# Kernel optimization log

Hardware: AMD Instinct MI355X
Metric: run time of the kernel (lower is better)

Reference implementation:

```python
import jax, jax.numpy as jnp
import numpy as np
import math

D_INPUT = 1024
D_Q = 1024
D_K = 1024
D_V = 1024
D_MODEL = 1024
B, S = 4, 2048


def setup_inputs() -> dict:
    key = jax.random.key(0)
    ks = jax.random.split(key, 9)
    sc = 0.02
    return {
        "x": jax.random.normal(ks[0], (B, S, D_INPUT), dtype=jnp.float32),
        "wq": jax.random.normal(ks[1], (D_INPUT, D_Q), dtype=jnp.float32) * sc,
        "bq": jnp.zeros((D_Q,), dtype=jnp.float32),
        "wk": jax.random.normal(ks[2], (D_INPUT, D_K), dtype=jnp.float32) * sc,
        "bk": jnp.zeros((D_K,), dtype=jnp.float32),
        "wv": jax.random.normal(ks[3], (D_INPUT, D_V), dtype=jnp.float32) * sc,
        "bv": jnp.zeros((D_V,), dtype=jnp.float32),
        "wp": jax.random.normal(ks[4], (D_V, D_MODEL), dtype=jnp.float32) * sc,
        "bp": jnp.zeros((D_MODEL,), dtype=jnp.float32),
    }


def reference(x, wq, bq, wk, bk, wv, bv, wp, bp):
    scale = math.sqrt(D_K)  # NOTE: original MULTIPLIES by sqrt(d_k)
    q = x @ wq + bq  # [B,S,Dq]
    k = x @ wk + bk  # [B,S,Dk]
    v = x @ wv + bv  # [B,S,Dv]
    scores = jnp.einsum('bsd,btd->bst', q, k) * scale
    p_attn = jax.nn.softmax(scores, axis=-1)
    # dropout: inference mode (training=False) -> identity
    context = jnp.einsum('bst,btd->bsd', p_attn, v)
    output = context @ wp + bp
    return (output, p_attn)
```

## Files before the change

### kernel.cpp

```cpp
#include <hip/hip_runtime.h>

typedef unsigned short u16;
typedef short bf16x8 __attribute__((ext_vector_type(8)));
typedef float floatx4 __attribute__((ext_vector_type(4)));

static __device__ __forceinline__ u16 f2bf(float f) {
  unsigned int u = __float_as_uint(f);
  unsigned int lsb = (u >> 16) & 1u;
  u += 0x7FFFu + lsb;
  return (u16)(u >> 16);
}
static __device__ __forceinline__ float bf2f(u16 u) {
  return __uint_as_float(((unsigned int)u) << 16);
}

static __device__ __forceinline__ void gl_lds16(const u16* g, u16* l) {
  __builtin_amdgcn_global_load_lds(
      (const __attribute__((address_space(1))) void*)g,
      (__attribute__((address_space(3))) void*)l, 16, 0, 0);
}

__global__ __launch_bounds__(256)
void prep_weights(const float* __restrict__ wq, const float* __restrict__ wk,
                  const float* __restrict__ wv, const float* __restrict__ wp,
                  const float* __restrict__ bq, const float* __restrict__ bk,
                  u16* __restrict__ qkvThi, u16* __restrict__ qkvTlo,
                  u16* __restrict__ wpThi, float* __restrict__ bqk) {
  __shared__ float t[32][33];
  const int z = blockIdx.z;
  const int tid = threadIdx.x;
  if (z == 4) {
    if (blockIdx.y == 0 && blockIdx.x < 8) {
      const int i = blockIdx.x * 256 + tid;
      bqk[i] = (i < 1024) ? bq[i] : bk[i - 1024];
    }
    return;
  }
  const float* in = (z == 0) ? wq : (z == 1) ? wk : (z == 2) ? wv : wp;
  u16* hi = (z == 3) ? wpThi : (qkvThi + (size_t)z * 1024 * 1024);
  u16* lo = (z == 0) ? qkvTlo : (z == 1) ? (qkvTlo + 1024 * 1024) : (u16*)nullptr;
  const int want_lo = (z < 2);

  const int r0 = blockIdx.y * 32, c0 = blockIdx.x * 32;
  const int lr = tid >> 3;
  const int lc = (tid & 7) * 4;
  float4 v = *(const float4*)(in + (size_t)(r0 + lr) * 1024 + c0 + lc);
  t[lr][lc + 0] = v.x; t[lr][lc + 1] = v.y; t[lr][lc + 2] = v.z; t[lr][lc + 3] = v.w;
  __syncthreads();
  u16 ph[4], pl[4];
#pragma unroll
  for (int j = 0; j < 4; j++) {
    float f = t[lc + j][lr];
    ph[j] = f2bf(f);
    pl[j] = f2bf(f - bf2f(ph[j]));
  }
  const size_t o = (size_t)(c0 + lr) * 1024 + r0 + lc;
  *(uint2*)(hi + o) = *(uint2*)ph;
  if (want_lo) *(uint2*)(lo + o) = *(uint2*)pl;
}

__global__ __launch_bounds__(256)
void split_f32(const float* __restrict__ in, u16* __restrict__ hi,
               u16* __restrict__ lo) {
  const size_t i4 = ((size_t)blockIdx.x * 256 + threadIdx.x) * 4;
  float4 v = *(const float4*)(in + i4);
  float f[4] = {v.x, v.y, v.z, v.w};
  u16 ph[4], pl[4];
#pragma unroll
  for (int j = 0; j < 4; j++) {
    ph[j] = f2bf(f[j]);
    pl[j] = f2bf(f[j] - bf2f(ph[j]));
  }
  *(uint2*)(hi + i4) = *(uint2*)ph;
  *(uint2*)(lo + i4) = *(uint2*)pl;
}

template<int KB, int ASP, int BSP, int OM, int HB>
__global__ __launch_bounds__(256)
void gemm_mfma(const u16* __restrict__ Ahi, const u16* __restrict__ Alo,
               const u16* __restrict__ Bhi, const u16* __restrict__ Blo,
               const float* __restrict__ bias,
               void* __restrict__ C0, void* __restrict__ C1,
               void* __restrict__ C2, void* __restrict__ C3,
               int N, int K, int lda, int ldb, int ldc,
               long long aB, long long bB, long long cB, float scale) {
  constexpr int CM = KB / 8 - 1;
  constexpr int RPI = 512 / KB;
  constexpr int NI = KB / 16;
  constexpr int PL = 128 * KB;
  __shared__ __align__(16) u16 As[(1 + ASP) * PL];
  __shared__ __align__(16) u16 Bs[(1 + BSP) * PL];

  const int bz = blockIdx.z;
  const u16* A0 = Ahi + (size_t)bz * aB;
  const u16* A1 = ASP ? (Alo + (size_t)bz * aB) : (const u16*)nullptr;
  const u16* B0 = Bhi + (size_t)bz * bB;
  const u16* B1 = BSP ? (Blo + (size_t)bz * bB) : (const u16*)nullptr;

  const int m0 = blockIdx.y * 128;
  const int n0 = blockIdx.x * 128;
  const int tid = threadIdx.x;
  const int w = tid >> 6;
  const int L = tid & 63;
  const int rr = L & 15, quad = L >> 4;
  const int wm = (w >> 1) * 64, wn = (w & 1) * 64;

  const int lrow = (KB == 32) ? (L >> 2) : (L >> 3);
  const int c3 = (L & CM) ^ ((L >> 3) & CM);
  const int srow = w * 32 + lrow;
  u16* stA = &As[w * 32 * KB];
  u16* stB = &Bs[w * 32 * KB];
  const u16* gA0 = A0 + (size_t)(m0 + srow) * lda + c3 * 8;
  const u16* gA1 = ASP ? A1 + (size_t)(m0 + srow) * lda + c3 * 8 : (const u16*)nullptr;
  const u16* gB0 = B0 + (size_t)(n0 + srow) * ldb + c3 * 8;
  const u16* gB1 = BSP ? B1 + (size_t)(n0 + srow) * ldb + c3 * 8 : (const u16*)nullptr;

  floatx4 acc[4][4] = {};

  for (int k0 = 0; k0 < K; k0 += KB) {
#pragma unroll
    for (int q = 0; q < NI; q++) {
      gl_lds16(gA0 + k0 + (size_t)q * RPI * lda, stA + q * 512);
      gl_lds16(gB0 + k0 + (size_t)q * RPI * ldb, stB + q * 512);
    }
    if (ASP) {
#pragma unroll
      for (int q = 0; q < NI; q++)
        gl_lds16(gA1 + k0 + (size_t)q * RPI * lda, stA + PL + q * 512);
    }
    if (BSP) {
#pragma unroll
      for (int q = 0; q < NI; q++)
        gl_lds16(gB1 + k0 + (size_t)q * RPI * ldb, stB + PL + q * 512);
    }
    __syncthreads();

#pragma unroll
    for (int s = 0; s < KB / 32; s++) {
      const int pcb = ((KB == 32) ? (quad ^ ((rr >> 1) & 3))
                                  : ((s * 4 + quad) ^ (rr & 7))) * 8;
      bf16x8 a0[4], a1[4], b0[4], b1[4];
#pragma unroll
      for (int i = 0; i < 4; i++) {
        const int arow = wm + i * 16 + rr;
        const int brow = wn + i * 16 + rr;
        a0[i] = *(const bf16x8*)&As[arow * KB + pcb];
        b0[i] = *(const bf16x8*)&Bs[brow * KB + pcb];
        if (ASP) a1[i] = *(const bf16x8*)&As[PL + arow * KB + pcb];
        if (BSP) b1[i] = *(const bf16x8*)&Bs[PL + brow * KB + pcb];
      }
#pragma unroll
      for (int i = 0; i < 4; i++) {
#pragma unroll
        for (int j = 0; j < 4; j++) {
          acc[i][j] = __builtin_amdgcn_mfma_f32_16x16x32_bf16(a0[i], b0[j], acc[i][j], 0, 0, 0);
          if (ASP && BSP) {
            acc[i][j] = __builtin_amdgcn_mfma_f32_16x16x32_bf16(a0[i], b1[j], acc[i][j], 0, 0, 0);
            acc[i][j] = __builtin_amdgcn_mfma_f32_16x16x32_bf16(a1[i], b0[j], acc[i][j], 0, 0, 0);
          }
        }
      }
    }
    __syncthreads();
  }

#pragma unroll
  for (int i = 0; i < 4; i++) {
    const int mbase = m0 + wm + i * 16 + quad * 4;
#pragma unroll
    for (int j = 0; j < 4; j++) {
      const int col = n0 + wn + j * 16 + rr;
      float bvs = 0.f;
      if (HB) bvs = bias[col];
      if (OM == 3) {
        u16 pk[4];
#pragma unroll
        for (int ii = 0; ii < 4; ii++) pk[ii] = f2bf(acc[i][j][ii] * scale + bvs);
        const size_t idx = (size_t)(mbase >> 11) * (2048 * 1024) +
                           (size_t)col * 2048 + (mbase & 2047);
        *(uint2*)((u16*)C0 + idx) = *(uint2*)pk;
      } else if (OM == 5) {
        u16* hi; u16* lo;
        if (col < 1024) { hi = (u16*)C0; lo = (u16*)C1; }
        else            { hi = (u16*)C2; lo = (u16*)C3; }
        const int cc = col & 1023;
#pragma unroll
        for (int ii = 0; ii < 4; ii++) {
          const float v = acc[i][j][ii] + bvs;
          const size_t idx = (size_t)(mbase + ii) * 1024 + cc;
          const u16 h = f2bf(v);
          hi[idx] = h;
          lo[idx] = f2bf(v - bf2f(h));
        }
      } else {
        u16* Cb = (u16*)C0 + (size_t)bz * cB;
        float* Cf = (float*)C0 + (size_t)bz * cB;
        u16* Cl = (OM == 1) ? ((u16*)C1 + (size_t)bz * cB) : (u16*)nullptr;
#pragma unroll
        for (int ii = 0; ii < 4; ii++) {
          const float v = acc[i][j][ii] * scale + bvs;
          const size_t idx = (size_t)(mbase + ii) * ldc + col;
          if (OM == 0) {
            Cb[idx] = f2bf(v);
          } else if (OM == 1) {
            const u16 h = f2bf(v);
            Cb[idx] = h;
            Cl[idx] = f2bf(v - bf2f(h));
          } else {
            Cf[idx] = v;
          }
        }
      }
    }
  }
}

__global__ __launch_bounds__(256)
void softmax_rows(float* __restrict__ S, u16* __restrict__ Pb) {
  const int row = blockIdx.x;
  float* s = S + (size_t)row * 2048;
  const int tid = threadIdx.x;
  const int w = tid >> 6;
  __shared__ float redm[4];
  __shared__ float reds[4];

  float v[8];
  float mx = -1e30f;
#pragma unroll
  for (int i = 0; i < 8; i++) {
    v[i] = s[tid + 256 * i];
    mx = fmaxf(mx, v[i]);
  }
#pragma unroll
  for (int o = 32; o > 0; o >>= 1) mx = fmaxf(mx, __shfl_xor(mx, o, 64));
  if ((tid & 63) == 0) redm[w] = mx;
  __syncthreads();
  mx = fmaxf(fmaxf(redm[0], redm[1]), fmaxf(redm[2], redm[3]));

  float sum = 0.f;
#pragma unroll
  for (int i = 0; i < 8; i++) {
    v[i] = __expf(v[i] - mx);
    sum += v[i];
  }
#pragma unroll
  for (int o = 32; o > 0; o >>= 1) sum += __shfl_xor(sum, o, 64);
  if ((tid & 63) == 0) reds[w] = sum;
  __syncthreads();
  sum = reds[0] + reds[1] + reds[2] + reds[3];
  const float rs = 1.0f / sum;
#pragma unroll
  for (int i = 0; i < 8; i++) {
    const float p = v[i] * rs;
    s[tid + 256 * i] = p;
    Pb[(size_t)row * 2048 + tid + 256 * i] = f2bf(p);
  }
}

extern "C" void kernel_launch(void* const* d_in, const int* in_sizes, int n_in,
                              void* d_out, int out_size, void* d_ws, size_t ws_size,
                              hipStream_t stream) {
  const float* x  = (const float*)d_in[0];
  const float* wq = (const float*)d_in[1];
  const float* bq = (const float*)d_in[2];
  const float* wk = (const float*)d_in[3];
  const float* bk = (const float*)d_in[4];
  const float* wv = (const float*)d_in[5];
  const float* bv = (const float*)d_in[6];
  const float* wp = (const float*)d_in[7];
  const float* bp = (const float*)d_in[8];

  const size_t MB = 1024 * 1024;
  char* ws = (char*)d_ws;
  u16* qkvThi = (u16*)(ws + 0 * MB);
  u16* qkvTlo = (u16*)(ws + 6 * MB);
  u16* wpThi  = (u16*)(ws + 10 * MB);
  float* bqk  = (float*)(ws + 12 * MB);
  u16* xhi    = (u16*)(ws + 13 * MB);
  u16* xlo    = (u16*)(ws + 29 * MB);
  u16* qhi    = (u16*)(ws + 45 * MB);
  u16* qlo    = (u16*)(ws + 61 * MB);
  u16* khi    = (u16*)(ws + 77 * MB);
  u16* klo    = (u16*)(ws + 93 * MB);
  u16* vT     = (u16*)(ws + 109 * MB);
  u16* pbf    = khi;
  u16* ctx    = qhi;

  float* outp = (float*)d_out;
  float* scf  = (float*)d_out + 8388608;

  const dim3 blk(256);

  prep_weights<<<dim3(32, 32, 5), blk, 0, stream>>>(
      wq, wk, wv, wp, bq, bk, qkvThi, qkvTlo, wpThi, bqk);
  split_f32<<<dim3(8192), blk, 0, stream>>>(x, xhi, xlo);

  gemm_mfma<32, 1, 1, 5, 1><<<dim3(16, 64, 1), blk, 0, stream>>>(
      xhi, xlo, qkvThi, qkvTlo, bqk, qhi, qlo, khi, klo,
      2048, 1024, 1024, 1024, 1024, 0, 0, 0, 1.0f);

  gemm_mfma<32, 0, 0, 3, 1><<<dim3(8, 64, 1), blk, 0, stream>>>(
      xhi, nullptr, qkvThi + 2 * 1024 * 1024, nullptr, bv, vT, nullptr, nullptr, nullptr,
      1024, 1024, 1024, 1024, 0, 0, 0, 0, 1.0f);

  gemm_mfma<32, 1, 1, 2, 0><<<dim3(16, 16, 4), blk, 0, stream>>>(
      qhi, qlo, khi, klo, nullptr, scf, nullptr, nullptr, nullptr,
      2048, 1024, 1024, 1024, 2048,
      2048LL * 1024, 2048LL * 1024, 2048LL * 2048, 32.0f);

  softmax_rows<<<dim3(8192), blk, 0, stream>>>(scf, pbf);

  gemm_mfma<64, 0, 0, 0, 0><<<dim3(8, 16, 4), blk, 0, stream>>>(
      pbf, nullptr, vT, nullptr, nullptr, ctx, nullptr, nullptr, nullptr,
      1024, 2048, 2048, 2048, 1024,
      2048LL * 2048, 1024LL * 2048, 2048LL * 1024, 1.0f);

  gemm_mfma<64, 0, 0, 2, 1><<<dim3(8, 64, 1), blk, 0, stream>>>(
      ctx, nullptr, wpThi, nullptr, bp, outp, nullptr, nullptr, nullptr,
      1024, 1024, 1024, 1024, 1024, 0, 0, 0, 1.0f);
}
```

Before: 501.2 us.

## Reassociate attention value path as (P·X)·Wv and fuse x split into prep

Uses the fact that softmax rows sum to one to compute context as (P·X)·Wv + bv instead of P·(X·Wv + bv). The prep kernel now also splits x into hi/lo and writes a bf16 transposed copy of x, replacing the separate split kernel and the V projection GEMM with an extra projection GEMM after P·X. This removes one kernel launch and the V-transpose epilogue, but adds an extra bf16 rounding of the intermediate P·X product.

```diff
diff --git a/kernel.cpp b/kernel.cpp
--- a/kernel.cpp
+++ b/kernel.cpp
@@ -21,14 +21,21 @@
 }
 
 __global__ __launch_bounds__(256)
-void prep_weights(const float* __restrict__ wq, const float* __restrict__ wk,
-                  const float* __restrict__ wv, const float* __restrict__ wp,
-                  const float* __restrict__ bq, const float* __restrict__ bk,
-                  u16* __restrict__ qkvThi, u16* __restrict__ qkvTlo,
-                  u16* __restrict__ wpThi, float* __restrict__ bqk) {
+void prep_all(const float* __restrict__ wq, const float* __restrict__ wk,
+              const float* __restrict__ wv, const float* __restrict__ wp,
+              const float* __restrict__ bq, const float* __restrict__ bk,
+              const float* __restrict__ x,
+              u16* __restrict__ qkThi, u16* __restrict__ qkTlo,
+              u16* __restrict__ wvThi, u16* __restrict__ wpThi,
+              float* __restrict__ bqk,
+              u16* __restrict__ xhi, u16* __restrict__ xlo,
+              u16* __restrict__ xThi) {
   __shared__ float t[32][33];
   const int z = blockIdx.z;
   const int tid = threadIdx.x;
+  const int lr = tid >> 3;
+  const int lc = (tid & 7) * 4;
+
   if (z == 4) {
     if (blockIdx.y == 0 && blockIdx.x < 8) {
       const int i = blockIdx.x * 256 + tid;
@@ -36,14 +43,38 @@
     }
     return;
   }
+
+  if (z >= 5) {
+    const int r0 = ((z - 5) * 32 + blockIdx.y) * 32;
+    const int c0 = blockIdx.x * 32;
+    float4 v = *(const float4*)(x + (size_t)(r0 + lr) * 1024 + c0 + lc);
+    float f[4] = {v.x, v.y, v.z, v.w};
+    t[lr][lc + 0] = v.x; t[lr][lc + 1] = v.y; t[lr][lc + 2] = v.z; t[lr][lc + 3] = v.w;
+    u16 ph[4], pl[4];
+#pragma unroll
+    for (int j = 0; j < 4; j++) {
+      ph[j] = f2bf(f[j]);
+      pl[j] = f2bf(f[j] - bf2f(ph[j]));
+    }
+    const size_t o = (size_t)(r0 + lr) * 1024 + c0 + lc;
+    *(uint2*)(xhi + o) = *(uint2*)ph;
+    *(uint2*)(xlo + o) = *(uint2*)pl;
+    __syncthreads();
+    u16 pt[4];
+#pragma unroll
+    for (int j = 0; j < 4; j++) pt[j] = f2bf(t[lc + j][lr]);
+    const int b = r0 >> 11, rt = r0 & 2047;
+    *(uint2*)(xThi + (size_t)b * (1024 * 2048) + (size_t)(c0 + lr) * 2048 + rt + lc) =
+        *(uint2*)pt;
+    return;
+  }
+
   const float* in = (z == 0) ? wq : (z == 1) ? wk : (z == 2) ? wv : wp;
-  u16* hi = (z == 3) ? wpThi : (qkvThi + (size_t)z * 1024 * 1024);
-  u16* lo = (z == 0) ? qkvTlo : (z == 1) ? (qkvTlo + 1024 * 1024) : (u16*)nullptr;
+  u16* hi = (z == 2) ? wvThi : (z == 3) ? wpThi : (qkThi + (size_t)z * 1024 * 1024);
+  u16* lo = (z == 0) ? qkTlo : (z == 1) ? (qkTlo + 1024 * 1024) : (u16*)nullptr;
   const int want_lo = (z < 2);
 
   const int r0 = blockIdx.y * 32, c0 = blockIdx.x * 32;
-  const int lr = tid >> 3;
-  const int lc = (tid & 7) * 4;
   float4 v = *(const float4*)(in + (size_t)(r0 + lr) * 1024 + c0 + lc);
   t[lr][lc + 0] = v.x; t[lr][lc + 1] = v.y; t[lr][lc + 2] = v.z; t[lr][lc + 3] = v.w;
   __syncthreads();
@@ -52,27 +83,11 @@
   for (int j = 0; j < 4; j++) {
     float f = t[lc + j][lr];
     ph[j] = f2bf(f);
-    pl[j] = f2bf(f - bf2f(ph[j]));
+    if (want_lo) pl[j] = f2bf(f - bf2f(ph[j]));
   }
   const size_t o = (size_t)(c0 + lr) * 1024 + r0 + lc;
   *(uint2*)(hi + o) = *(uint2*)ph;
   if (want_lo) *(uint2*)(lo + o) = *(uint2*)pl;
-}
-
-__global__ __launch_bounds__(256)
-void split_f32(const float* __restrict__ in, u16* __restrict__ hi,
-               u16* __restrict__ lo) {
-  const size_t i4 = ((size_t)blockIdx.x * 256 + threadIdx.x) * 4;
-  float4 v = *(const float4*)(in + i4);
-  float f[4] = {v.x, v.y, v.z, v.w};
-  u16 ph[4], pl[4];
-#pragma unroll
-  for (int j = 0; j < 4; j++) {
-    ph[j] = f2bf(f[j]);
-    pl[j] = f2bf(f[j] - bf2f(ph[j]));
-  }
-  *(uint2*)(hi + i4) = *(uint2*)ph;
-  *(uint2*)(lo + i4) = *(uint2*)pl;
 }
 
 template<int KB, int ASP, int BSP, int OM, int HB>
@@ -172,14 +187,7 @@
       const int col = n0 + wn + j * 16 + rr;
       float bvs = 0.f;
       if (HB) bvs = bias[col];
-      if (OM == 3) {
-        u16 pk[4];
-#pragma unroll
-        for (int ii = 0; ii < 4; ii++) pk[ii] = f2bf(acc[i][j][ii] * scale + bvs);
-        const size_t idx = (size_t)(mbase >> 11) * (2048 * 1024) +
-                           (size_t)col * 2048 + (mbase & 2047);
-        *(uint2*)((u16*)C0 + idx) = *(uint2*)pk;
-      } else if (OM == 5) {
+      if (OM == 5) {
         u16* hi; u16* lo;
         if (col < 1024) { hi = (u16*)C0; lo = (u16*)C1; }
         else            { hi = (u16*)C2; lo = (u16*)C3; }
@@ -272,36 +280,33 @@
 
   const size_t MB = 1024 * 1024;
   char* ws = (char*)d_ws;
-  u16* qkvThi = (u16*)(ws + 0 * MB);
-  u16* qkvTlo = (u16*)(ws + 6 * MB);
-  u16* wpThi  = (u16*)(ws + 10 * MB);
-  float* bqk  = (float*)(ws + 12 * MB);
-  u16* xhi    = (u16*)(ws + 13 * MB);
-  u16* xlo    = (u16*)(ws + 29 * MB);
-  u16* qhi    = (u16*)(ws + 45 * MB);
-  u16* qlo    = (u16*)(ws + 61 * MB);
-  u16* khi    = (u16*)(ws + 77 * MB);
-  u16* klo    = (u16*)(ws + 93 * MB);
-  u16* vT     = (u16*)(ws + 109 * MB);
-  u16* pbf    = khi;
-  u16* ctx    = qhi;
+  u16* qkThi = (u16*)(ws + 0 * MB);
+  u16* qkTlo = (u16*)(ws + 4 * MB);
+  u16* wvThi = (u16*)(ws + 8 * MB);
+  u16* wpThi = (u16*)(ws + 10 * MB);
+  float* bqk = (float*)(ws + 12 * MB);
+  u16* xhi   = (u16*)(ws + 13 * MB);
+  u16* xlo   = (u16*)(ws + 29 * MB);
+  u16* qhi   = (u16*)(ws + 45 * MB);
+  u16* qlo   = (u16*)(ws + 61 * MB);
+  u16* khi   = (u16*)(ws + 77 * MB);
+  u16* klo   = (u16*)(ws + 93 * MB);
+  u16* xThi  = (u16*)(ws + 109 * MB);
+  u16* pbf   = khi;
+  u16* px    = qhi;
+  u16* ctx   = qlo;
 
   float* outp = (float*)d_out;
   float* scf  = (float*)d_out + 8388608;
 
   const dim3 blk(256);
 
-  prep_weights<<<dim3(32, 32, 5), blk, 0, stream>>>(
-      wq, wk, wv, wp, bq, bk, qkvThi, qkvTlo, wpThi, bqk);
-  split_f32<<<dim3(8192), blk, 0, stream>>>(x, xhi, xlo);
+  prep_all<<<dim3(32, 32, 13), blk, 0, stream>>>(
+      wq, wk, wv, wp, bq, bk, x, qkThi, qkTlo, wvThi, wpThi, bqk, xhi, xlo, xThi);
 
   gemm_mfma<32, 1, 1, 5, 1><<<dim3(16, 64, 1), blk, 0, stream>>>(
-      xhi, xlo, qkvThi, qkvTlo, bqk, qhi, qlo, khi, klo,
+      xhi, xlo, qkThi, qkTlo, bqk, qhi, qlo, khi, klo,
       2048, 1024, 1024, 1024, 1024, 0, 0, 0, 1.0f);
-
-  gemm_mfma<32, 0, 0, 3, 1><<<dim3(8, 64, 1), blk, 0, stream>>>(
-      xhi, nullptr, qkvThi + 2 * 1024 * 1024, nullptr, bv, vT, nullptr, nullptr, nullptr,
-      1024, 1024, 1024, 1024, 0, 0, 0, 0, 1.0f);
 
   gemm_mfma<32, 1, 1, 2, 0><<<dim3(16, 16, 4), blk, 0, stream>>>(
       qhi, qlo, khi, klo, nullptr, scf, nullptr, nullptr, nullptr,
@@ -311,9 +316,13 @@
   softmax_rows<<<dim3(8192), blk, 0, stream>>>(scf, pbf);
 
   gemm_mfma<64, 0, 0, 0, 0><<<dim3(8, 16, 4), blk, 0, stream>>>(
-      pbf, nullptr, vT, nullptr, nullptr, ctx, nullptr, nullptr, nullptr,
+      pbf, nullptr, xThi, nullptr, nullptr, px, nullptr, nullptr, nullptr,
       1024, 2048, 2048, 2048, 1024,
       2048LL * 2048, 1024LL * 2048, 2048LL * 1024, 1.0f);
+
+  gemm_mfma<64, 0, 0, 0, 1><<<dim3(8, 64, 1), blk, 0, stream>>>(
+      px, nullptr, wvThi, nullptr, bv, ctx, nullptr, nullptr, nullptr,
+      1024, 1024, 1024, 1024, 1024, 0, 0, 0, 1.0f);
 
   gemm_mfma<64, 0, 0, 2, 1><<<dim3(8, 64, 1), blk, 0, stream>>>(
       ctx, nullptr, wpThi, nullptr, bp, outp, nullptr, nullptr, nullptr,
```

Measured after the change: 476.6 us. 1.05x faster.
